# Kernel optimization log

Measured on AMD Instinct MI355X. Metric: run time of the kernel, lower is better.

The kernel has to match this reference:

```python
import jax, jax.numpy as jnp
import numpy as np

A, B, D = 64, 128, 256   # batch, route nodes, feature_dim
H, C = 64, 32            # hidden_capsule, center_num
NUM_ITERS = 3


def _squash(t, axis=-1):
    sq = jnp.sum(t * t, axis=axis, keepdims=True)
    return (sq / (1.0 + sq)) * t / jnp.sqrt(sq)


def _route(priors, n_iters):
    # priors: [K, A, R, D]; dynamic routing over axis=2 (R).
    # Original keeps logits of priors' full shape, but they stay constant
    # along D (init zeros, delta has keepdim on last axis), so [K,A,R,1]
    # is exactly equivalent and avoids a redundant [K,A,R,D] buffer.
    logits = jnp.zeros(priors.shape[:-1] + (1,), priors.dtype)
    outputs = None
    for i in range(n_iters):
        probs = jax.nn.softmax(logits, axis=2)          # [K,A,R,1]
        outputs = _squash(jnp.sum(probs * priors, axis=2, keepdims=True))  # [K,A,1,D]
        if i != n_iters - 1:
            logits = logits + jnp.sum(priors * outputs, axis=-1, keepdims=True)
    return outputs


def setup_inputs() -> dict:
    key = jax.random.key(0)
    k1, k2, k3 = jax.random.split(key, 3)
    x = jax.random.normal(k1, (A, B, D), dtype=jnp.float32)
    route_weights1 = jax.random.normal(k2, (H, D, D), dtype=jnp.float32)
    route_weights = jax.random.normal(k3, (C, D, D), dtype=jnp.float32)
    return {"x": x, "route_weights1": route_weights1, "route_weights": route_weights}


def reference(x, route_weights1, route_weights):
    # stage 1: priors1[h,a,b,:] = x[a,b,:] @ W1[h]  -> [H,A,B,D]
    priors1 = jnp.einsum('abd,hde->habe', x, route_weights1)
    out1 = _route(priors1, NUM_ITERS)                  # [H,A,1,D]
    out1 = jnp.transpose(out1[:, :, 0, :], (1, 0, 2))  # squeeze + transpose(0,1) -> [A,H,D]
    # stage 2: priors[c,a,h,:] = out1[a,h,:] @ W[c]   -> [C,A,H,D]
    priors = jnp.einsum('ahd,cde->cahe', out1, route_weights)
    out = _route(priors, NUM_ITERS)                    # [C,A,1,D]
    return out[:, :, 0, :]                             # squeeze -> [C,A,D]
```

## Files before the change

### kernel.cpp

```cpp
#include <hip/hip_runtime.h>
#include <hip/hip_bf16.h>

typedef __attribute__((ext_vector_type(8))) short bf16x8;
typedef __attribute__((ext_vector_type(4))) float f32x4;
typedef unsigned short u16;
typedef unsigned int u32;

__device__ __forceinline__ u32 bf16_rne(float f) {
  u32 u = __float_as_uint(f);
  return (u + 0x7FFFu + ((u >> 16) & 1u)) >> 16;
}
__device__ __forceinline__ float bf16_val(u32 b) { return __uint_as_float(b << 16); }

__device__ __forceinline__ void g2l16(const u16* g, u16* l) {
  __builtin_amdgcn_global_load_lds(
      (const __attribute__((address_space(1))) u32*)g,
      (__attribute__((address_space(3))) u32*)l, 16, 0, 0);
}

__global__ void split_arr(const float* __restrict__ in,
                          u16* __restrict__ hi, u16* __restrict__ lo, int n4) {
  int i = blockIdx.x * 256 + threadIdx.x;
  if (i >= n4) return;
  float4 v = ((const float4*)in)[i];
  u32 h0 = bf16_rne(v.x), h1 = bf16_rne(v.y), h2 = bf16_rne(v.z), h3 = bf16_rne(v.w);
  u32 l0 = bf16_rne(v.x - bf16_val(h0));
  u32 l1 = bf16_rne(v.y - bf16_val(h1));
  u32 l2 = bf16_rne(v.z - bf16_val(h2));
  u32 l3 = bf16_rne(v.w - bf16_val(h3));
  ushort4 hv; hv.x = (u16)h0; hv.y = (u16)h1; hv.z = (u16)h2; hv.w = (u16)h3;
  ushort4 lv; lv.x = (u16)l0; lv.y = (u16)l1; lv.z = (u16)l2; lv.w = (u16)l3;
  ((ushort4*)hi)[i] = hv;
  ((ushort4*)lo)[i] = lv;
}

__global__ void split_transpose256(const float* __restrict__ in,
                                   u16* __restrict__ hi, u16* __restrict__ lo) {
  __shared__ float tile[32][33];
  const size_t off = (size_t)blockIdx.z * 65536;
  const int tx = threadIdx.x, ty = threadIdx.y;
#pragma unroll
  for (int i = 0; i < 4; ++i) {
    int y = blockIdx.y * 32 + ty + i * 8;
    int x = blockIdx.x * 32 + tx;
    tile[ty + i * 8][tx] = in[off + (size_t)y * 256 + x];
  }
  __syncthreads();
#pragma unroll
  for (int i = 0; i < 4; ++i) {
    float v = tile[tx][ty + i * 8];
    u32 hb = bf16_rne(v);
    u32 lb = bf16_rne(v - bf16_val(hb));
    size_t idx = off + (size_t)(blockIdx.x * 32 + ty + i * 8) * 256 + blockIdx.y * 32 + tx;
    hi[idx] = (u16)hb;
    lo[idx] = (u16)lb;
  }
}

template <int R>
__global__ __launch_bounds__(512, 2) void caps_route(
    const u16* __restrict__ Ahi_g,
    const u16* __restrict__ Alo_g,
    const u16* __restrict__ Whi,
    const u16* __restrict__ Wlo,
    u16* __restrict__ o1hi, u16* __restrict__ o1lo,
    float* __restrict__ outp,
    int KN, int stage) {
  constexpr int APB = 256 / R;
  constexpr int SEG = APB / 2;
  constexpr int MTS = 8 / SEG;
  constexpr int ABS = (R == 128) ? 5 : 4;
  __shared__ u16 BUF[2][32768];
  __shared__ __align__(16) float wlog[4][256];
  __shared__ __align__(16) float probs[256];
  __shared__ float sqpart[4][4];

  const int tid = threadIdx.x;
  const int w = tid >> 6, lane = tid & 63, q = lane >> 4, li = lane & 15;
  const int mg = w >> 2, eg = w & 3;
  const int kk = blockIdx.x >> ABS;
  const int ab = blockIdx.x & ((1 << ABS) - 1);

  const int sub = lane >> 2, p = lane & 3;
  const int gslot = p ^ ((sub >> 1) & 3);
  const size_t goff = (size_t)w * 4096 + sub * 256 + gslot * 8;
  const u16* gAh = Ahi_g + (size_t)ab * 65536 + goff;
  const u16* gAl = Alo_g + (size_t)ab * 65536 + goff;
  const u16* gWh = Whi  + (size_t)kk * 65536 + goff;
  const u16* gWl = Wlo  + (size_t)kk * 65536 + goff;
  u16* l0 = &BUF[0][0] + w * 512 + lane * 8;
  u16* l1 = &BUF[1][0] + w * 512 + lane * 8;

#define STAGE8(ko, l)                          \
  do {                                         \
    g2l16(gAh + (ko), (l));                    \
    g2l16(gAh + (ko) + 32768, (l) + 4096);     \
    g2l16(gAl + (ko), (l) + 8192);             \
    g2l16(gAl + (ko) + 32768, (l) + 12288);    \
    g2l16(gWh + (ko), (l) + 16384);            \
    g2l16(gWh + (ko) + 32768, (l) + 20480);    \
    g2l16(gWl + (ko), (l) + 24576);            \
    g2l16(gWl + (ko) + 32768, (l) + 28672);    \
  } while (0)

  const int rslot = q ^ ((li >> 1) & 3);
  const int fbase = li * 32 + rslot * 8;

  f32x4 acc[8][4] = {};

  STAGE8(0, l0);

#pragma unroll
  for (int ks = 0; ks < 8; ++ks) {
    const u16* B0 = (ks & 1) ? &BUF[1][0] : &BUF[0][0];
    if (ks < 7) {
      const int ko = (ks + 1) * 32;
      if (ks & 1) STAGE8(ko, l0); else STAGE8(ko, l1);
      asm volatile("s_waitcnt vmcnt(8)" ::: "memory");
    } else {
      asm volatile("s_waitcnt vmcnt(0)" ::: "memory");
    }
    __builtin_amdgcn_s_barrier();
    asm volatile("" ::: "memory");
    bf16x8 bh[4], bl[4];
#pragma unroll
    for (int ct = 0; ct < 4; ++ct) {
      const u16* bp = B0 + 16384 + (eg * 4 + ct) * 512 + fbase;
      bh[ct] = *(const bf16x8*)bp;
      bl[ct] = *(const bf16x8*)(bp + 8192);
    }
#pragma unroll
    for (int mt = 0; mt < 8; ++mt) {
      const u16* ap = B0 + (mg * 8 + mt) * 512 + fbase;
      bf16x8 ah = *(const bf16x8*)ap;
      bf16x8 al = *(const bf16x8*)(ap + 8192);
#pragma unroll
      for (int ct = 0; ct < 4; ++ct) {
        acc[mt][ct] = __builtin_amdgcn_mfma_f32_16x16x32_bf16(al, bh[ct], acc[mt][ct], 0, 0, 0);
        acc[mt][ct] = __builtin_amdgcn_mfma_f32_16x16x32_bf16(ah, bl[ct], acc[mt][ct], 0, 0, 0);
        acc[mt][ct] = __builtin_amdgcn_mfma_f32_16x16x32_bf16(ah, bh[ct], acc[mt][ct], 0, 0, 0);
      }
    }
    asm volatile("" ::: "memory");
    __builtin_amdgcn_s_barrier();
  }
#undef STAGE8

  const float invR = 1.0f / R;
  float v[SEG][4];
  float lg0 = 0.f, lg1 = 0.f;

  for (int iter = 0; iter < 3; ++iter) {
    float s[SEG][4];
#pragma unroll
    for (int sg = 0; sg < SEG; ++sg) {
#pragma unroll
      for (int ct = 0; ct < 4; ++ct) {
        float t = 0.f;
#pragma unroll
        for (int mi = 0; mi < MTS; ++mi) {
          const int mt = sg * MTS + mi;
          float4 p4;
          if (iter == 0) { p4.x = invR; p4.y = invR; p4.z = invR; p4.w = invR; }
          else           p4 = *(const float4*)&probs[mg * 128 + mt * 16 + q * 4];
          t += p4.x * acc[mt][ct][0] + p4.y * acc[mt][ct][1] +
               p4.z * acc[mt][ct][2] + p4.w * acc[mt][ct][3];
        }
        t += __shfl_xor(t, 16);
        t += __shfl_xor(t, 32);
        s[sg][ct] = t;
      }
    }
#pragma unroll
    for (int sg = 0; sg < SEG; ++sg) {
      float ss = s[sg][0] * s[sg][0] + s[sg][1] * s[sg][1] +
                 s[sg][2] * s[sg][2] + s[sg][3] * s[sg][3];
      ss += __shfl_xor(ss, 1); ss += __shfl_xor(ss, 2);
      ss += __shfl_xor(ss, 4); ss += __shfl_xor(ss, 8);
      if (lane == 0) sqpart[mg * SEG + sg][eg] = ss;
    }
    __syncthreads();
#pragma unroll
    for (int sg = 0; sg < SEG; ++sg) {
      const int a = mg * SEG + sg;
      float sq = sqpart[a][0] + sqpart[a][1] + sqpart[a][2] + sqpart[a][3];
      float scale = (sq > 0.f) ? sq / ((1.0f + sq) * sqrtf(sq)) : 0.f;
#pragma unroll
      for (int ct = 0; ct < 4; ++ct) v[sg][ct] = s[sg][ct] * scale;
    }

    if (iter < 2) {
#pragma unroll
      for (int mt = 0; mt < 8; ++mt) {
        const int sg = mt / MTS;
        float tt[4];
#pragma unroll
        for (int rr = 0; rr < 4; ++rr) {
          float t = acc[mt][0][rr] * v[sg][0] + acc[mt][1][rr] * v[sg][1] +
                    acc[mt][2][rr] * v[sg][2] + acc[mt][3][rr] * v[sg][3];
          t += __shfl_xor(t, 1); t += __shfl_xor(t, 2);
          t += __shfl_xor(t, 4); t += __shfl_xor(t, 8);
          tt[rr] = t;
        }
        if (li == 0)
          *(float4*)&wlog[eg][mg * 128 + mt * 16 + q * 4] =
              make_float4(tt[0], tt[1], tt[2], tt[3]);
      }
      __syncthreads();
      if (w < APB) {
        if (R == 128) {
          int r0 = w * 128 + lane, r1 = r0 + 64;
          lg0 += wlog[0][r0] + wlog[1][r0] + wlog[2][r0] + wlog[3][r0];
          lg1 += wlog[0][r1] + wlog[1][r1] + wlog[2][r1] + wlog[3][r1];
          float m = fmaxf(lg0, lg1);
#pragma unroll
          for (int d2 = 1; d2 < 64; d2 <<= 1) m = fmaxf(m, __shfl_xor(m, d2));
          float e0 = expf(lg0 - m), e1 = expf(lg1 - m);
          float zz = e0 + e1;
#pragma unroll
          for (int d2 = 1; d2 < 64; d2 <<= 1) zz += __shfl_xor(zz, d2);
          float inv = 1.0f / zz;
          probs[r0] = e0 * inv;
          probs[r1] = e1 * inv;
        } else {
          int r0 = w * 64 + lane;
          lg0 += wlog[0][r0] + wlog[1][r0] + wlog[2][r0] + wlog[3][r0];
          float m = lg0;
#pragma unroll
          for (int d2 = 1; d2 < 64; d2 <<= 1) m = fmaxf(m, __shfl_xor(m, d2));
          float e0 = expf(lg0 - m);
          float zz = e0;
#pragma unroll
          for (int d2 = 1; d2 < 64; d2 <<= 1) zz += __shfl_xor(zz, d2);
          probs[r0] = e0 / zz;
        }
      }
      __syncthreads();
    }
  }

  if (q == 0) {
#pragma unroll
    for (int sg = 0; sg < SEG; ++sg) {
      const int ag = ab * APB + mg * SEG + sg;
      if (stage == 1) {
        size_t ob = ((size_t)ag * KN + kk) * 256;
#pragma unroll
        for (int ct = 0; ct < 4; ++ct) {
          int e = eg * 64 + ct * 16 + li;
          u32 hb = bf16_rne(v[sg][ct]);
          u32 lb = bf16_rne(v[sg][ct] - bf16_val(hb));
          o1hi[ob + e] = (u16)hb;
          o1lo[ob + e] = (u16)lb;
        }
      } else {
        size_t ob = ((size_t)kk * 64 + ag) * 256;
#pragma unroll
        for (int ct = 0; ct < 4; ++ct) {
          int e = eg * 64 + ct * 16 + li;
          outp[ob + e] = v[sg][ct];
        }
      }
    }
  }
}

extern "C" void kernel_launch(void* const* d_in, const int* in_sizes, int n_in,
                              void* d_out, int out_size, void* d_ws, size_t ws_size,
                              hipStream_t stream) {
  const float* x  = (const float*)d_in[0];
  const float* w1 = (const float*)d_in[1];
  const float* wc = (const float*)d_in[2];
  float* out = (float*)d_out;

  char* ws = (char*)d_ws;
  u16* w1hi = (u16*)(ws);
  u16* w1lo = (u16*)(ws + (8u << 20));
  u16* wchi = (u16*)(ws + (16u << 20));
  u16* wclo = (u16*)(ws + (20u << 20));
  u16* xhi  = (u16*)(ws + (24u << 20));
  u16* xlo  = (u16*)(ws + (28u << 20));
  u16* o1hi = (u16*)(ws + (32u << 20));
  u16* o1lo = (u16*)(ws + (34u << 20));

  split_arr<<<2048, 256, 0, stream>>>(x, xhi, xlo, 524288);
  split_transpose256<<<dim3(8, 8, 64), dim3(32, 8), 0, stream>>>(w1, w1hi, w1lo);
  split_transpose256<<<dim3(8, 8, 32), dim3(32, 8), 0, stream>>>(wc, wchi, wclo);
  caps_route<128><<<64 * 32, 512, 0, stream>>>(xhi, xlo, w1hi, w1lo, o1hi, o1lo, nullptr, 64, 1);
  caps_route<64><<<32 * 16, 512, 0, stream>>>(o1hi, o1lo, wchi, wclo, nullptr, nullptr, out, 32, 2);
}
```

Before: 360.5 us.

## Prefetch A fragments, group MFMAs by pass, and drop softmax barrier

In the MFMA inner loop, the next A-tile fragments are loaded from LDS while the current tile's MFMAs run. The MFMAs are grouped by bf16 split pass and wrapped in s_setprio to raise wave priority. The routing softmax now runs in every wave on its own row block instead of only the first APB waves. This removes the trailing __syncthreads in favour of an LDS waitcnt, and probs are hoisted into registers before the reduction and expf becomes __expf. The aim is to hide LDS latency and cut block-wide barriers, at the risk of cross-wave races on probs/wlog if the row ownership assumption is wrong.

```diff
diff --git a/kernel.cpp b/kernel.cpp
--- a/kernel.cpp
+++ b/kernel.cpp
@@ -129,17 +129,28 @@
       bh[ct] = *(const bf16x8*)bp;
       bl[ct] = *(const bf16x8*)(bp + 8192);
     }
+    const u16* aB = B0 + mg * 4096 + fbase;
+    bf16x8 ahc = *(const bf16x8*)(aB);
+    bf16x8 alc = *(const bf16x8*)(aB + 8192);
 #pragma unroll
     for (int mt = 0; mt < 8; ++mt) {
-      const u16* ap = B0 + (mg * 8 + mt) * 512 + fbase;
-      bf16x8 ah = *(const bf16x8*)ap;
-      bf16x8 al = *(const bf16x8*)(ap + 8192);
-#pragma unroll
-      for (int ct = 0; ct < 4; ++ct) {
-        acc[mt][ct] = __builtin_amdgcn_mfma_f32_16x16x32_bf16(al, bh[ct], acc[mt][ct], 0, 0, 0);
-        acc[mt][ct] = __builtin_amdgcn_mfma_f32_16x16x32_bf16(ah, bl[ct], acc[mt][ct], 0, 0, 0);
-        acc[mt][ct] = __builtin_amdgcn_mfma_f32_16x16x32_bf16(ah, bh[ct], acc[mt][ct], 0, 0, 0);
-      }
+      bf16x8 ahn, aln;
+      if (mt < 7) {
+        ahn = *(const bf16x8*)(aB + (mt + 1) * 512);
+        aln = *(const bf16x8*)(aB + (mt + 1) * 512 + 8192);
+      }
+      __builtin_amdgcn_s_setprio(1);
+#pragma unroll
+      for (int ct = 0; ct < 4; ++ct)
+        acc[mt][ct] = __builtin_amdgcn_mfma_f32_16x16x32_bf16(alc, bh[ct], acc[mt][ct], 0, 0, 0);
+#pragma unroll
+      for (int ct = 0; ct < 4; ++ct)
+        acc[mt][ct] = __builtin_amdgcn_mfma_f32_16x16x32_bf16(ahc, bl[ct], acc[mt][ct], 0, 0, 0);
+#pragma unroll
+      for (int ct = 0; ct < 4; ++ct)
+        acc[mt][ct] = __builtin_amdgcn_mfma_f32_16x16x32_bf16(ahc, bh[ct], acc[mt][ct], 0, 0, 0);
+      __builtin_amdgcn_s_setprio(0);
+      if (mt < 7) { ahc = ahn; alc = aln; }
     }
     asm volatile("" ::: "memory");
     __builtin_amdgcn_s_barrier();
@@ -147,10 +158,22 @@
 #undef STAGE8
 
   const float invR = 1.0f / R;
+  const int rb = mg * 128;
   float v[SEG][4];
   float lg0 = 0.f, lg1 = 0.f;
 
   for (int iter = 0; iter < 3; ++iter) {
+    float4 p4[8];
+    if (iter == 0) {
+#pragma unroll
+      for (int mt = 0; mt < 8; ++mt) {
+        p4[mt].x = invR; p4[mt].y = invR; p4[mt].z = invR; p4[mt].w = invR;
+      }
+    } else {
+#pragma unroll
+      for (int mt = 0; mt < 8; ++mt)
+        p4[mt] = *(const float4*)&probs[rb + mt * 16 + q * 4];
+    }
     float s[SEG][4];
 #pragma unroll
     for (int sg = 0; sg < SEG; ++sg) {
@@ -160,11 +183,8 @@
 #pragma unroll
         for (int mi = 0; mi < MTS; ++mi) {
           const int mt = sg * MTS + mi;
-          float4 p4;
-          if (iter == 0) { p4.x = invR; p4.y = invR; p4.z = invR; p4.w = invR; }
-          else           p4 = *(const float4*)&probs[mg * 128 + mt * 16 + q * 4];
-          t += p4.x * acc[mt][ct][0] + p4.y * acc[mt][ct][1] +
-               p4.z * acc[mt][ct][2] + p4.w * acc[mt][ct][3];
+          t += p4[mt].x * acc[mt][ct][0] + p4[mt].y * acc[mt][ct][1] +
+               p4[mt].z * acc[mt][ct][2] + p4[mt].w * acc[mt][ct][3];
         }
         t += __shfl_xor(t, 16);
         t += __shfl_xor(t, 32);
@@ -203,39 +223,45 @@
           tt[rr] = t;
         }
         if (li == 0)
-          *(float4*)&wlog[eg][mg * 128 + mt * 16 + q * 4] =
+          *(float4*)&wlog[eg][rb + mt * 16 + q * 4] =
               make_float4(tt[0], tt[1], tt[2], tt[3]);
       }
       __syncthreads();
-      if (w < APB) {
-        if (R == 128) {
-          int r0 = w * 128 + lane, r1 = r0 + 64;
-          lg0 += wlog[0][r0] + wlog[1][r0] + wlog[2][r0] + wlog[3][r0];
-          lg1 += wlog[0][r1] + wlog[1][r1] + wlog[2][r1] + wlog[3][r1];
-          float m = fmaxf(lg0, lg1);
-#pragma unroll
-          for (int d2 = 1; d2 < 64; d2 <<= 1) m = fmaxf(m, __shfl_xor(m, d2));
-          float e0 = expf(lg0 - m), e1 = expf(lg1 - m);
-          float zz = e0 + e1;
-#pragma unroll
-          for (int d2 = 1; d2 < 64; d2 <<= 1) zz += __shfl_xor(zz, d2);
-          float inv = 1.0f / zz;
-          probs[r0] = e0 * inv;
-          probs[r1] = e1 * inv;
-        } else {
-          int r0 = w * 64 + lane;
-          lg0 += wlog[0][r0] + wlog[1][r0] + wlog[2][r0] + wlog[3][r0];
-          float m = lg0;
-#pragma unroll
-          for (int d2 = 1; d2 < 64; d2 <<= 1) m = fmaxf(m, __shfl_xor(m, d2));
-          float e0 = expf(lg0 - m);
-          float zz = e0;
-#pragma unroll
-          for (int d2 = 1; d2 < 64; d2 <<= 1) zz += __shfl_xor(zz, d2);
-          probs[r0] = e0 / zz;
-        }
-      }
-      __syncthreads();
+      if (R == 128) {
+        int r0 = rb + lane, r1 = r0 + 64;
+        lg0 += wlog[0][r0] + wlog[1][r0] + wlog[2][r0] + wlog[3][r0];
+        lg1 += wlog[0][r1] + wlog[1][r1] + wlog[2][r1] + wlog[3][r1];
+        float m = fmaxf(lg0, lg1);
+#pragma unroll
+        for (int d2 = 1; d2 < 64; d2 <<= 1) m = fmaxf(m, __shfl_xor(m, d2));
+        float e0 = __expf(lg0 - m), e1 = __expf(lg1 - m);
+        float zz = e0 + e1;
+#pragma unroll
+        for (int d2 = 1; d2 < 64; d2 <<= 1) zz += __shfl_xor(zz, d2);
+        float inv = 1.0f / zz;
+        probs[r0] = e0 * inv;
+        probs[r1] = e1 * inv;
+      } else {
+        int r0 = rb + lane, r1 = r0 + 64;
+        lg0 += wlog[0][r0] + wlog[1][r0] + wlog[2][r0] + wlog[3][r0];
+        lg1 += wlog[0][r1] + wlog[1][r1] + wlog[2][r1] + wlog[3][r1];
+        float m0 = lg0, m1 = lg1;
+#pragma unroll
+        for (int d2 = 1; d2 < 64; d2 <<= 1) {
+          m0 = fmaxf(m0, __shfl_xor(m0, d2));
+          m1 = fmaxf(m1, __shfl_xor(m1, d2));
+        }
+        float e0 = __expf(lg0 - m0), e1 = __expf(lg1 - m1);
+        float z0 = e0, z1 = e1;
+#pragma unroll
+        for (int d2 = 1; d2 < 64; d2 <<= 1) {
+          z0 += __shfl_xor(z0, d2);
+          z1 += __shfl_xor(z1, d2);
+        }
+        probs[r0] = e0 / z0;
+        probs[r1] = e1 / z1;
+      }
+      asm volatile("s_waitcnt lgkmcnt(0)" ::: "memory");
     }
   }
 
```

Measured after the change: 373.7 us. 1.04x slower.
